# Performance work log

Hardware: AMD Instinct MI355X
Metric: run time of the kernel (lower is better)

## Reference

```python
import jax, jax.numpy as jnp
import numpy as np

B, S, E, H = 2, 2048, 1024, 16
HD = E // H            # head_dim = 64
ROT = 64               # rotary_dim == head_dim
BASE = 10000.0


def setup_inputs() -> dict:
    key = jax.random.key(0)
    k1, k2, k3, k4, k5 = jax.random.split(key, 5)
    return {
        "x": jax.random.normal(k1, (B, S, E), dtype=jnp.float32),
        "mask": jnp.ones((B, S), dtype=jnp.int32),
        "qkv_w": jax.random.normal(k2, (3 * E, E), dtype=jnp.float32) * (1.0 / np.sqrt(E)),
        "qkv_b": jax.random.normal(k3, (3 * E,), dtype=jnp.float32) * 0.02,
        "out_w": jax.random.normal(k4, (E, E), dtype=jnp.float32) * (1.0 / np.sqrt(E)),
        "out_b": jax.random.normal(k5, (E,), dtype=jnp.float32) * 0.02,
    }


def _rotate_half(x):
    # split last dim into (even, odd) pairs and rotate 90 degrees
    x = x.reshape(*x.shape[:-1], -1, 2)
    x1, x2 = x[..., 0], x[..., 1]
    return jnp.stack((-x2, x1), axis=-1).reshape(*x.shape[:-2], -1)


def _rope_cos_sin(seq_len, rot_dim, dtype):
    inv_freq = 1.0 / (BASE ** (jnp.arange(0, rot_dim, 2, dtype=jnp.float32) / rot_dim))
    freqs = jnp.arange(seq_len, dtype=jnp.float32)[:, None] * inv_freq[None, :]  # [S, rot/2]
    cos = jnp.repeat(jnp.cos(freqs), 2, axis=-1).astype(dtype)  # [S, rot]
    sin = jnp.repeat(jnp.sin(freqs), 2, axis=-1).astype(dtype)
    return cos, sin


def reference(x, mask, qkv_w, qkv_b, out_w, out_b):
    b, s, _ = x.shape
    qkv = x @ qkv_w.T + qkv_b                      # [B,S,3E]
    q, k, v = jnp.split(qkv, 3, axis=-1)
    shape = lambda t: t.reshape(b, s, H, HD).transpose(0, 2, 1, 3)  # [B,H,S,HD]
    q, k, v = shape(q), shape(k), shape(v)

    cos, sin = _rope_cos_sin(s, ROT, q.dtype)      # [S, ROT]
    cos = cos[None, None]                          # [1,1,S,ROT]
    sin = sin[None, None]
    q_rot, q_pass = q[..., :ROT], q[..., ROT:]
    k_rot, k_pass = k[..., :ROT], k[..., ROT:]
    q = jnp.concatenate((q_rot * cos + _rotate_half(q_rot) * sin, q_pass), axis=-1)
    k = jnp.concatenate((k_rot * cos + _rotate_half(k_rot) * sin, k_pass), axis=-1)

    scale = 1.0 / np.sqrt(HD)
    scores = jnp.einsum("bhqd,bhkd->bhqk", q, k) * scale  # [B,H,S,S]
    keep = (mask != 0)[:, None, None, :]           # [B,1,1,S]
    scores = jnp.where(keep, scores, -jnp.inf)
    attn = jax.nn.softmax(scores, axis=-1)
    context = jnp.einsum("bhqk,bhkd->bhqd", attn, v)
    context = context.transpose(0, 2, 1, 3).reshape(b, s, E)
    return context @ out_w.T + out_b
```

## Files before the change

kernel.cpp:

```cpp
#include <hip/hip_runtime.h>
#include <hip/hip_bf16.h>
#include <cmath>

#define SB 2048
#define EB 1024
#define NH 16
#define HD 64
#define KLOG 0.14391156831212788f
#define QSC 0.18033688011112042f

typedef unsigned short u16;
typedef unsigned int u32;
typedef __attribute__((ext_vector_type(8))) short short8;
typedef __attribute__((ext_vector_type(4))) float f32x4;

__device__ __forceinline__ u16 f2b(float x) {
  __hip_bfloat16 h = __float2bfloat16(x);
  return *reinterpret_cast<u16*>(&h);
}

__device__ __forceinline__ u32 pkb(float lo, float hi) {
#if __has_builtin(__builtin_amdgcn_cvt_pk_bf16_f32)
  auto v = __builtin_amdgcn_cvt_pk_bf16_f32(lo, hi);
  u32 r;
  __builtin_memcpy(&r, &v, 4);
  return r;
#else
  return (u32)f2b(lo) | ((u32)f2b(hi) << 16);
#endif
}

__device__ __forceinline__ void gl_lds16(const u16* g, u16* l) {
  __builtin_amdgcn_global_load_lds(
      (const __attribute__((address_space(1))) unsigned int*)g,
      (__attribute__((address_space(3))) unsigned int*)l, 16, 0, 0);
}

#define CN1 (4096 * 1024 / 4)
#define CN2 (3072 * 1024 / 4)
#define CN3 (1024 * 1024 / 4)
#define CNS (CN1 + CN2 + CN3)
__global__ __launch_bounds__(256) void conv_all(
    const float* __restrict__ x, const float* __restrict__ w1,
    const float* __restrict__ w2, const int* __restrict__ mask,
    u16* __restrict__ xb, u16* __restrict__ wqb, u16* __restrict__ owb,
    float* __restrict__ ctab, float* __restrict__ stab,
    float* __restrict__ fbias) {
  int i = blockIdx.x * 256 + threadIdx.x;
  if (i < CNS) {
    const float* src;
    u16* dst;
    int j;
    if (i < CN1) { src = x; dst = xb; j = i; }
    else if (i < CN1 + CN2) { src = w1; dst = wqb; j = i - CN1; }
    else { src = w2; dst = owb; j = i - CN1 - CN2; }
    float4 v = ((const float4*)src)[j];
    ushort4 o;
    o.x = f2b(v.x); o.y = f2b(v.y); o.z = f2b(v.z); o.w = f2b(v.w);
    ((ushort4*)dst)[j] = o;
  } else {
    int j = i - CNS;
    if (j < SB * 32) {
      int pos = j >> 5, p = j & 31;
      float th = (float)pos * expf(-(float)(2 * p) * KLOG);
      float sn, cs;
      sincosf(th, &sn, &cs);
      ctab[j] = cs; stab[j] = sn;
    } else {
      int j2 = j - SB * 32;
      if (j2 < 2 * SB) fbias[j2] = mask[j2] ? 0.f : -1e9f;
    }
  }
}

__global__ __launch_bounds__(256) void qkv_mfma_rope(
    const u16* __restrict__ A, const u16* __restrict__ Bw,
    const float* __restrict__ bias, const float* __restrict__ ctab,
    const float* __restrict__ stab, u16* __restrict__ qb,
    u16* __restrict__ kb, u16* __restrict__ vt) {
  __shared__ u16 As[128 * 32];
  __shared__ u16 Bs[128 * 32];
  __shared__ float CS[128 * 32];
  __shared__ float SN[128 * 32];

  const int t = threadIdx.x;
  const int lane = t & 63, wv = t >> 6;
  const int l15 = lane & 15, quad = lane >> 4;
  const int wm = wv >> 1, wn = wv & 1;
  const int m0 = blockIdx.x * 128;
  const int n0 = blockIdx.y * 128;

  f32x4 acc[4][4] = {};

  for (int k0 = 0; k0 < 1024; k0 += 32) {
#pragma unroll
    for (int c = 0; c < 2; c++) {
      int r = wv * 32 + c * 16;
      const u16* ga = A + (size_t)(m0 + r + (lane >> 2)) * 1024 + k0 + (lane & 3) * 8;
      const u16* gb = Bw + (size_t)(n0 + r + (lane >> 2)) * 1024 + k0 + (lane & 3) * 8;
      gl_lds16(ga, &As[r * 32]);
      gl_lds16(gb, &Bs[r * 32]);
    }
    __syncthreads();

    short8 a[4], b[4];
#pragma unroll
    for (int mi = 0; mi < 4; mi++)
      a[mi] = *(const short8*)&As[(wm * 64 + mi * 16 + l15) * 32 + quad * 8];
#pragma unroll
    for (int ni = 0; ni < 4; ni++)
      b[ni] = *(const short8*)&Bs[(wn * 64 + ni * 16 + l15) * 32 + quad * 8];
#pragma unroll
    for (int mi = 0; mi < 4; mi++)
#pragma unroll
      for (int ni = 0; ni < 4; ni++)
        acc[mi][ni] = __builtin_amdgcn_mfma_f32_16x16x32_bf16(a[mi], b[ni], acc[mi][ni], 0, 0, 0);
    __syncthreads();
  }

  const int n_base = n0 + wn * 64;
  const int which = n_base >> 10;
  float b4[4];
#pragma unroll
  for (int ni = 0; ni < 4; ni++) b4[ni] = bias[n_base + ni * 16 + l15];

  {
    int base = (m0 & 2047) * 32;
#pragma unroll
    for (int i = 0; i < 4; i++) {
      int idx = (t + i * 256) * 4;
      *(float4*)&CS[idx] = *(const float4*)&ctab[base + idx];
      *(float4*)&SN[idx] = *(const float4*)&stab[base + idx];
    }
  }
  __syncthreads();

  const int h = (n_base & 1023) >> 6;
  const int bb = m0 >> 11;
  if (which < 2) {
    u16* dst = (which == 0) ? qb : kb;
#pragma unroll
    for (int mi = 0; mi < 4; mi++) {
#pragma unroll
      for (int r = 0; r < 4; r++) {
        int row = wm * 64 + mi * 16 + quad * 4 + r;
        int s = (m0 & 2047) + row;
        size_t obase = ((size_t)(bb * NH + h) * SB + s) * HD;
#pragma unroll
        for (int ni = 0; ni < 4; ni++) {
          float v = acc[mi][ni][r] + b4[ni];
          int d = ni * 16 + l15;
          float pv = __shfl_xor(v, 1, 64);
          float c = CS[row * 32 + (d >> 1)];
          float sn_ = SN[row * 32 + (d >> 1)];
          v = v * c + pv * ((d & 1) ? sn_ : -sn_);
          if (which == 0) v *= QSC;
          dst[obase + d] = f2b(v);
        }
      }
    }
  } else {
    size_t tbase = (size_t)(bb * NH + h) * HD;
#pragma unroll
    for (int mi = 0; mi < 4; mi++) {
      int s0 = (m0 & 2047) + wm * 64 + mi * 16 + quad * 4;
#pragma unroll
      for (int ni = 0; ni < 4; ni++) {
        int d = ni * 16 + l15;
        u32 p0 = pkb(acc[mi][ni][0] + b4[ni], acc[mi][ni][1] + b4[ni]);
        u32 p1 = pkb(acc[mi][ni][2] + b4[ni], acc[mi][ni][3] + b4[ni]);
        uint2 pk = make_uint2(p0, p1);
        *(uint2*)&vt[(tbase + d) * SB + s0] = pk;
      }
    }
  }
}

__global__ __launch_bounds__(512, 4) void attn_mfma(
    const u16* __restrict__ qb, const u16* __restrict__ kb,
    const u16* __restrict__ vt, const float* __restrict__ fbias,
    u16* __restrict__ ctx) {
  __shared__ u16 Ks[2][4096];
  __shared__ u16 Vt[2][4096];
  __shared__ u32 Ps2[8][16][34];

  const int bh = blockIdx.x, b = bh >> 4, h = bh & 15;
  const int q0 = blockIdx.y * 128;
  const int t = threadIdx.x;
  const int lane = t & 63, wv = t >> 6;
  const int l15 = lane & 15, quad = lane >> 4;

  short8 bq[2];
  {
    const u16* qp = qb + ((size_t)bh * SB + q0 + wv * 16 + l15) * HD;
    bq[0] = *(const short8*)&qp[quad * 8];
    bq[1] = *(const short8*)&qp[32 + quad * 8];
  }

  const u16* kbase = kb + (size_t)bh * SB * HD;
  const u16* vbase = vt + (size_t)bh * HD * SB;
  const float* fbase = fbias + b * SB;

  const int srow = lane >> 3;
  const int schunk = ((lane & 7) ^ srow) * 8;
  const int fslot = quad ^ (l15 & 7);

  gl_lds16(kbase + (size_t)(wv * 8 + srow) * HD + schunk, &Ks[0][wv * 512]);
  gl_lds16(vbase + (size_t)(wv * 8 + srow) * SB + schunk, &Vt[0][wv * 512]);

  f32x4 o[4] = {};
  float l_i = 0.f;

  for (int kt = 0; kt < SB / 64; kt++) {
    const int bufi = kt & 1;
    __syncthreads();

    if (kt + 1 < SB / 64) {
      size_t ko = (size_t)(kt + 1) * 64;
      gl_lds16(kbase + (ko + wv * 8 + srow) * HD + schunk, &Ks[1 - bufi][wv * 512]);
      gl_lds16(vbase + (size_t)(wv * 8 + srow) * SB + ko + schunk, &Vt[1 - bufi][wv * 512]);
    }

    f32x4 s[4];
#pragma unroll
    for (int mb = 0; mb < 4; mb++) {
      const u16* kr = &Ks[bufi][(mb * 16 + l15) * 64];
      short8 a0 = *(const short8*)&kr[fslot * 8];
      short8 a1 = *(const short8*)&kr[(fslot ^ 4) * 8];
      f32x4 z = {};
      z = __builtin_amdgcn_mfma_f32_16x16x32_bf16(a0, bq[0], z, 0, 0, 0);
      s[mb] = __builtin_amdgcn_mfma_f32_16x16x32_bf16(a1, bq[1], z, 0, 0, 0);
    }

#pragma unroll
    for (int mb = 0; mb < 4; mb++) {
      f32x4 bias4 = *(const f32x4*)&fbase[kt * 64 + mb * 16 + quad * 4];
#pragma unroll
      for (int r = 0; r < 4; r++) {
        float p = __builtin_amdgcn_exp2f(s[mb][r] + bias4[r]);
        s[mb][r] = p;
        l_i += p;
      }
    }

#pragma unroll
    for (int mb = 0; mb < 4; mb++) {
      uint2 w2 = make_uint2(pkb(s[mb][0], s[mb][1]), pkb(s[mb][2], s[mb][3]));
      *(uint2*)&Ps2[wv][l15][8 * mb + 2 * quad] = w2;
    }
    short8 pb[2];
#pragma unroll
    for (int kk = 0; kk < 2; kk++)
      pb[kk] = *(const short8*)&Ps2[wv][l15][kk * 16 + 4 * quad];

#pragma unroll
    for (int nb = 0; nb < 4; nb++) {
      const u16* vr = &Vt[bufi][(nb * 16 + l15) * 64];
      short8 v0 = *(const short8*)&vr[fslot * 8];
      short8 v1 = *(const short8*)&vr[(fslot ^ 4) * 8];
      o[nb] = __builtin_amdgcn_mfma_f32_16x16x32_bf16(v0, pb[0], o[nb], 0, 0, 0);
      o[nb] = __builtin_amdgcn_mfma_f32_16x16x32_bf16(v1, pb[1], o[nb], 0, 0, 0);
    }
  }

  l_i += __shfl_xor(l_i, 16, 64);
  l_i += __shfl_xor(l_i, 32, 64);

  {
    float linv = 1.f / l_i;
    int qrow = q0 + wv * 16 + l15;
    size_t base = ((size_t)b * SB + qrow) * EB + h * HD;
#pragma unroll
    for (int nb = 0; nb < 4; nb++)
#pragma unroll
      for (int pr = 0; pr < 2; pr++) {
        int d = nb * 16 + quad * 4 + 2 * pr;
        *(u32*)&ctx[base + d] =
            pkb(o[nb][2 * pr] * linv, o[nb][2 * pr + 1] * linv);
      }
  }
}

__global__ __launch_bounds__(256) void out_mfma(
    const u16* __restrict__ A, const u16* __restrict__ Bw,
    const float* __restrict__ bias, float* __restrict__ out) {
  __shared__ u16 As[64 * 32];
  __shared__ u16 Bs[128 * 32];

  const int t = threadIdx.x;
  const int lane = t & 63, wv = t >> 6;
  const int l15 = lane & 15, quad = lane >> 4;
  const int wm = wv >> 1, wn = wv & 1;
  const int m0 = blockIdx.x * 64;
  const int n0 = blockIdx.y * 128;

  f32x4 acc[2][4] = {};

  for (int k0 = 0; k0 < 1024; k0 += 32) {
    {
      const u16* ga = A + (size_t)(m0 + wv * 16 + (lane >> 2)) * 1024 + k0 + (lane & 3) * 8;
      gl_lds16(ga, &As[(wv * 16) * 32]);
#pragma unroll
      for (int c = 0; c < 2; c++) {
        int r = wv * 32 + c * 16;
        const u16* gb = Bw + (size_t)(n0 + r + (lane >> 2)) * 1024 + k0 + (lane & 3) * 8;
        gl_lds16(gb, &Bs[r * 32]);
      }
    }
    __syncthreads();

    short8 a[2], b[4];
#pragma unroll
    for (int mi = 0; mi < 2; mi++)
      a[mi] = *(const short8*)&As[(wm * 32 + mi * 16 + l15) * 32 + quad * 8];
#pragma unroll
    for (int ni = 0; ni < 4; ni++)
      b[ni] = *(const short8*)&Bs[(wn * 64 + ni * 16 + l15) * 32 + quad * 8];
#pragma unroll
    for (int mi = 0; mi < 2; mi++)
#pragma unroll
      for (int ni = 0; ni < 4; ni++)
        acc[mi][ni] = __builtin_amdgcn_mfma_f32_16x16x32_bf16(a[mi], b[ni], acc[mi][ni], 0, 0, 0);
    __syncthreads();
  }

  float b4[4];
#pragma unroll
  for (int ni = 0; ni < 4; ni++) b4[ni] = bias[n0 + wn * 64 + ni * 16 + l15];
#pragma unroll
  for (int mi = 0; mi < 2; mi++)
#pragma unroll
    for (int r = 0; r < 4; r++) {
      int m = m0 + wm * 32 + mi * 16 + quad * 4 + r;
#pragma unroll
      for (int ni = 0; ni < 4; ni++)
        out[(size_t)m * 1024 + n0 + wn * 64 + ni * 16 + l15] = acc[mi][ni][r] + b4[ni];
    }
}

extern "C" void kernel_launch(void* const* d_in, const int* in_sizes, int n_in,
                              void* d_out, int out_size, void* d_ws, size_t ws_size,
                              hipStream_t stream) {
  const float* x     = (const float*)d_in[0];
  const int* mask    = (const int*)d_in[1];
  const float* qkv_w = (const float*)d_in[2];
  const float* qkv_b = (const float*)d_in[3];
  const float* out_w = (const float*)d_in[4];
  const float* out_b = (const float*)d_in[5];
  float* out = (float*)d_out;

  char* wsb = (char*)d_ws;
  u16* xb    = (u16*)wsb;
  u16* wqb   = (u16*)(wsb + ( 8ull << 20));
  u16* owb   = (u16*)(wsb + (14ull << 20));
  u16* qb    = (u16*)(wsb + (16ull << 20));
  u16* kb    = (u16*)(wsb + (24ull << 20));
  u16* vtb   = (u16*)(wsb + (32ull << 20));
  u16* cxb   = (u16*)(wsb + (40ull << 20));
  float* ctab = (float*)(wsb + (48ull << 20));
  float* stab = (float*)(wsb + (48ull << 20) + (256u << 10));
  float* fbias = (float*)(wsb + (48ull << 20) + (512u << 10));

  dim3 blk(256);
  int convBlocks = (CNS + SB * 32 + 2 * SB + 255) / 256;
  hipLaunchKernelGGL(conv_all, dim3(convBlocks), blk, 0, stream,
                     x, qkv_w, out_w, mask, xb, wqb, owb, ctab, stab, fbias);

  hipLaunchKernelGGL(qkv_mfma_rope, dim3(32, 24), blk, 0, stream,
                     xb, wqb, qkv_b, ctab, stab, qb, kb, vtb);

  hipLaunchKernelGGL(attn_mfma, dim3(32, 16), dim3(512), 0, stream,
                     qb, kb, vtb, fbias, cxb);

  hipLaunchKernelGGL(out_mfma, dim3(64, 8), blk, 0, stream, cxb, owb, out_b, out);
}
```

Before: 212.4 us.

## Split attention over two key halves with 32 queries per wave and combine

Each wave of the attention kernel now handles two 16-row query tiles, so every K/V tile loaded into LDS feeds twice as many MFMAs. The key sequence is split into two halves across blockIdx.z, which keeps the block count the same while each block covers 256 query rows. Each half writes a normalized partial context plus its row sum, and a new combine kernel merges them with sum weights before the output projection. This adds an extra kernel launch, an intermediate round trip through memory, and higher register pressure in exchange for better operand reuse. The second partial buffer reuses the xb workspace region, relying on xb not being needed after the QKV projection.

```diff
diff --git a/kernel.cpp b/kernel.cpp
--- a/kernel.cpp
+++ b/kernel.cpp
@@ -17,6 +17,13 @@
 __device__ __forceinline__ u16 f2b(float x) {
   __hip_bfloat16 h = __float2bfloat16(x);
   return *reinterpret_cast<u16*>(&h);
+}
+
+__device__ __forceinline__ float b2f(u16 v) {
+  u32 x = (u32)v << 16;
+  float f;
+  __builtin_memcpy(&f, &x, 4);
+  return f;
 }
 
 __device__ __forceinline__ u32 pkb(float lo, float hi) {
@@ -179,27 +186,29 @@
 __global__ __launch_bounds__(512, 4) void attn_mfma(
     const u16* __restrict__ qb, const u16* __restrict__ kb,
     const u16* __restrict__ vt, const float* __restrict__ fbias,
-    u16* __restrict__ ctx) {
+    u16* __restrict__ po0, u16* __restrict__ po1, float* __restrict__ pl) {
   __shared__ u16 Ks[2][4096];
   __shared__ u16 Vt[2][4096];
   __shared__ u32 Ps2[8][16][34];
 
-  const int bh = blockIdx.x, b = bh >> 4, h = bh & 15;
-  const int q0 = blockIdx.y * 128;
+  const int bh = blockIdx.x, b = bh >> 4;
+  const int q0 = blockIdx.y * 256;
+  const int kz = blockIdx.z;
   const int t = threadIdx.x;
   const int lane = t & 63, wv = t >> 6;
   const int l15 = lane & 15, quad = lane >> 4;
 
-  short8 bq[2];
-  {
-    const u16* qp = qb + ((size_t)bh * SB + q0 + wv * 16 + l15) * HD;
-    bq[0] = *(const short8*)&qp[quad * 8];
-    bq[1] = *(const short8*)&qp[32 + quad * 8];
-  }
-
-  const u16* kbase = kb + (size_t)bh * SB * HD;
-  const u16* vbase = vt + (size_t)bh * HD * SB;
-  const float* fbase = fbias + b * SB;
+  short8 bq[2][2];
+#pragma unroll
+  for (int qh = 0; qh < 2; qh++) {
+    const u16* qp = qb + ((size_t)bh * SB + q0 + wv * 32 + qh * 16 + l15) * HD;
+    bq[qh][0] = *(const short8*)&qp[quad * 8];
+    bq[qh][1] = *(const short8*)&qp[32 + quad * 8];
+  }
+
+  const u16* kbase = kb + (size_t)bh * SB * HD + (size_t)kz * 1024 * HD;
+  const u16* vbase = vt + (size_t)bh * HD * SB + kz * 1024;
+  const float* fbase = fbias + b * SB + kz * 1024;
 
   const int srow = lane >> 3;
   const int schunk = ((lane & 7) ^ srow) * 8;
@@ -208,28 +217,30 @@
   gl_lds16(kbase + (size_t)(wv * 8 + srow) * HD + schunk, &Ks[0][wv * 512]);
   gl_lds16(vbase + (size_t)(wv * 8 + srow) * SB + schunk, &Vt[0][wv * 512]);
 
-  f32x4 o[4] = {};
-  float l_i = 0.f;
-
-  for (int kt = 0; kt < SB / 64; kt++) {
+  f32x4 o[2][4] = {};
+  float l_i[2] = {0.f, 0.f};
+
+  for (int kt = 0; kt < 16; kt++) {
     const int bufi = kt & 1;
     __syncthreads();
 
-    if (kt + 1 < SB / 64) {
+    if (kt + 1 < 16) {
       size_t ko = (size_t)(kt + 1) * 64;
       gl_lds16(kbase + (ko + wv * 8 + srow) * HD + schunk, &Ks[1 - bufi][wv * 512]);
       gl_lds16(vbase + (size_t)(wv * 8 + srow) * SB + ko + schunk, &Vt[1 - bufi][wv * 512]);
     }
 
-    f32x4 s[4];
+    f32x4 s0[4], s1[4];
 #pragma unroll
     for (int mb = 0; mb < 4; mb++) {
       const u16* kr = &Ks[bufi][(mb * 16 + l15) * 64];
       short8 a0 = *(const short8*)&kr[fslot * 8];
       short8 a1 = *(const short8*)&kr[(fslot ^ 4) * 8];
-      f32x4 z = {};
-      z = __builtin_amdgcn_mfma_f32_16x16x32_bf16(a0, bq[0], z, 0, 0, 0);
-      s[mb] = __builtin_amdgcn_mfma_f32_16x16x32_bf16(a1, bq[1], z, 0, 0, 0);
+      f32x4 z0 = {}, z1 = {};
+      z0 = __builtin_amdgcn_mfma_f32_16x16x32_bf16(a0, bq[0][0], z0, 0, 0, 0);
+      s0[mb] = __builtin_amdgcn_mfma_f32_16x16x32_bf16(a1, bq[0][1], z0, 0, 0, 0);
+      z1 = __builtin_amdgcn_mfma_f32_16x16x32_bf16(a0, bq[1][0], z1, 0, 0, 0);
+      s1[mb] = __builtin_amdgcn_mfma_f32_16x16x32_bf16(a1, bq[1][1], z1, 0, 0, 0);
     }
 
 #pragma unroll
@@ -237,48 +248,82 @@
       f32x4 bias4 = *(const f32x4*)&fbase[kt * 64 + mb * 16 + quad * 4];
 #pragma unroll
       for (int r = 0; r < 4; r++) {
-        float p = __builtin_amdgcn_exp2f(s[mb][r] + bias4[r]);
-        s[mb][r] = p;
-        l_i += p;
+        float p0 = __builtin_amdgcn_exp2f(s0[mb][r] + bias4[r]);
+        float p1 = __builtin_amdgcn_exp2f(s1[mb][r] + bias4[r]);
+        s0[mb][r] = p0; l_i[0] += p0;
+        s1[mb][r] = p1; l_i[1] += p1;
       }
     }
 
+    short8 pb0[2], pb1[2];
 #pragma unroll
     for (int mb = 0; mb < 4; mb++) {
-      uint2 w2 = make_uint2(pkb(s[mb][0], s[mb][1]), pkb(s[mb][2], s[mb][3]));
+      uint2 w2 = make_uint2(pkb(s0[mb][0], s0[mb][1]), pkb(s0[mb][2], s0[mb][3]));
       *(uint2*)&Ps2[wv][l15][8 * mb + 2 * quad] = w2;
     }
-    short8 pb[2];
 #pragma unroll
     for (int kk = 0; kk < 2; kk++)
-      pb[kk] = *(const short8*)&Ps2[wv][l15][kk * 16 + 4 * quad];
+      pb0[kk] = *(const short8*)&Ps2[wv][l15][kk * 16 + 4 * quad];
+#pragma unroll
+    for (int mb = 0; mb < 4; mb++) {
+      uint2 w2 = make_uint2(pkb(s1[mb][0], s1[mb][1]), pkb(s1[mb][2], s1[mb][3]));
+      *(uint2*)&Ps2[wv][l15][8 * mb + 2 * quad] = w2;
+    }
+#pragma unroll
+    for (int kk = 0; kk < 2; kk++)
+      pb1[kk] = *(const short8*)&Ps2[wv][l15][kk * 16 + 4 * quad];
 
 #pragma unroll
     for (int nb = 0; nb < 4; nb++) {
       const u16* vr = &Vt[bufi][(nb * 16 + l15) * 64];
       short8 v0 = *(const short8*)&vr[fslot * 8];
       short8 v1 = *(const short8*)&vr[(fslot ^ 4) * 8];
-      o[nb] = __builtin_amdgcn_mfma_f32_16x16x32_bf16(v0, pb[0], o[nb], 0, 0, 0);
-      o[nb] = __builtin_amdgcn_mfma_f32_16x16x32_bf16(v1, pb[1], o[nb], 0, 0, 0);
-    }
-  }
-
-  l_i += __shfl_xor(l_i, 16, 64);
-  l_i += __shfl_xor(l_i, 32, 64);
-
-  {
-    float linv = 1.f / l_i;
-    int qrow = q0 + wv * 16 + l15;
-    size_t base = ((size_t)b * SB + qrow) * EB + h * HD;
+      o[0][nb] = __builtin_amdgcn_mfma_f32_16x16x32_bf16(v0, pb0[0], o[0][nb], 0, 0, 0);
+      o[0][nb] = __builtin_amdgcn_mfma_f32_16x16x32_bf16(v1, pb0[1], o[0][nb], 0, 0, 0);
+      o[1][nb] = __builtin_amdgcn_mfma_f32_16x16x32_bf16(v0, pb1[0], o[1][nb], 0, 0, 0);
+      o[1][nb] = __builtin_amdgcn_mfma_f32_16x16x32_bf16(v1, pb1[1], o[1][nb], 0, 0, 0);
+    }
+  }
+
+  u16* po = kz ? po1 : po0;
+#pragma unroll
+  for (int qh = 0; qh < 2; qh++) {
+    float l = l_i[qh];
+    l += __shfl_xor(l, 16, 64);
+    l += __shfl_xor(l, 32, 64);
+    float linv = 1.f / fmaxf(l, 1e-30f);
+    int qrow = q0 + wv * 32 + qh * 16 + l15;
+    size_t base = ((size_t)bh * SB + qrow) * HD;
 #pragma unroll
     for (int nb = 0; nb < 4; nb++)
 #pragma unroll
       for (int pr = 0; pr < 2; pr++) {
         int d = nb * 16 + quad * 4 + 2 * pr;
-        *(u32*)&ctx[base + d] =
-            pkb(o[nb][2 * pr] * linv, o[nb][2 * pr + 1] * linv);
+        *(u32*)&po[base + d] =
+            pkb(o[qh][nb][2 * pr] * linv, o[qh][nb][2 * pr + 1] * linv);
       }
-  }
+    if (quad == 0) pl[kz * (32 * SB) + bh * SB + qrow] = l;
+  }
+}
+
+__global__ __launch_bounds__(256) void combine(
+    const u16* __restrict__ po0, const u16* __restrict__ po1,
+    const float* __restrict__ pl, u16* __restrict__ ctx) {
+  int i = blockIdx.x * 256 + threadIdx.x;
+  int bh = i >> 16;
+  int r = i & 65535;
+  int qrow = r >> 5;
+  int dp = r & 31;
+  u32 ua = ((const u32*)po0)[i];
+  u32 ub = ((const u32*)po1)[i];
+  float l0 = pl[bh * SB + qrow];
+  float l1 = pl[32 * SB + bh * SB + qrow];
+  float rinv = 1.f / fmaxf(l0 + l1, 1e-30f);
+  float w0 = l0 * rinv, w1 = l1 * rinv;
+  float o0 = b2f((u16)(ua & 0xffff)) * w0 + b2f((u16)(ub & 0xffff)) * w1;
+  float o1 = b2f((u16)(ua >> 16)) * w0 + b2f((u16)(ub >> 16)) * w1;
+  int b = bh >> 4, h = bh & 15;
+  ((u32*)ctx)[(size_t)(b * SB + qrow) * 512 + h * 32 + dp] = pkb(o0, o1);
 }
 
 __global__ __launch_bounds__(256) void out_mfma(
@@ -357,9 +402,12 @@
   u16* kb    = (u16*)(wsb + (24ull << 20));
   u16* vtb   = (u16*)(wsb + (32ull << 20));
   u16* cxb   = (u16*)(wsb + (40ull << 20));
-  float* ctab = (float*)(wsb + (48ull << 20));
-  float* stab = (float*)(wsb + (48ull << 20) + (256u << 10));
-  float* fbias = (float*)(wsb + (48ull << 20) + (512u << 10));
+  u16* po1   = (u16*)(wsb + (48ull << 20));
+  float* ctab  = (float*)(wsb + (56ull << 20));
+  float* stab  = (float*)(wsb + (56ull << 20) + (256u << 10));
+  float* fbias = (float*)(wsb + (56ull << 20) + (512u << 10));
+  float* pl    = (float*)(wsb + (56ull << 20) + (768u << 10));
+  u16* po0   = xb;
 
   dim3 blk(256);
   int convBlocks = (CNS + SB * 32 + 2 * SB + 255) / 256;
@@ -369,8 +417,10 @@
   hipLaunchKernelGGL(qkv_mfma_rope, dim3(32, 24), blk, 0, stream,
                      xb, wqb, qkv_b, ctab, stab, qb, kb, vtb);
 
-  hipLaunchKernelGGL(attn_mfma, dim3(32, 16), dim3(512), 0, stream,
-                     qb, kb, vtb, fbias, cxb);
+  hipLaunchKernelGGL(attn_mfma, dim3(32, 8, 2), dim3(512), 0, stream,
+                     qb, kb, vtb, fbias, po0, po1, pl);
+
+  hipLaunchKernelGGL(combine, dim3(8192), blk, 0, stream, po0, po1, pl, cxb);
 
   hipLaunchKernelGGL(out_mfma, dim3(64, 8), blk, 0, stream, cxb, owb, out_b, out);
 }
```

After: 207.1 us. -2.5%, faster.
